# Performance work log

Measured on AMD Instinct MI355X. Metric: run time of the kernel, lower is better.

## Reference

```python
import jax, jax.numpy as jnp
import numpy as np

VOCAB, BLOCK, C, H, L = 65, 60, 384, 6, 6
HS = C // H  # 64
EPS = 1e-5


def _ln(x, g, b):
    mu = jnp.mean(x, axis=-1, keepdims=True)
    var = jnp.mean(jnp.square(x - mu), axis=-1, keepdims=True)
    return (x - mu) * jax.lax.rsqrt(var + EPS) * g + b


def setup_inputs() -> dict:
    key = jax.random.key(0)
    ks = jax.random.split(key, 16)
    std = 0.02
    B, T = 2048, 60
    inp = {
        'context': jax.random.randint(ks[0], (B, T), 0, VOCAB),
        'tok_emb': std * jax.random.normal(ks[1], (VOCAB, C), jnp.float32),
        'pos_emb': std * jax.random.normal(ks[2], (BLOCK, C), jnp.float32),
        # per-head projections stacked: [L, H, C, HS]
        'wq': std * jax.random.normal(ks[3], (L, H, C, HS), jnp.float32),
        'wk': std * jax.random.normal(ks[4], (L, H, C, HS), jnp.float32),
        'wv': std * jax.random.normal(ks[5], (L, H, C, HS), jnp.float32),
        'wo': std * jax.random.normal(ks[6], (L, C, C), jnp.float32),
        'bo': jnp.zeros((L, C), jnp.float32),
        'ln1_g': jnp.ones((L, C), jnp.float32),
        'ln1_b': jnp.zeros((L, C), jnp.float32),
        'ln2_g': jnp.ones((L, C), jnp.float32),
        'ln2_b': jnp.zeros((L, C), jnp.float32),
        'w1': std * jax.random.normal(ks[7], (L, C, 4 * C), jnp.float32),
        'b1': jnp.zeros((L, 4 * C), jnp.float32),
        'w2': std * jax.random.normal(ks[8], (L, 4 * C, C), jnp.float32),
        'b2': jnp.zeros((L, C), jnp.float32),
        'lnf_g': jnp.ones((C,), jnp.float32),
        'lnf_b': jnp.zeros((C,), jnp.float32),
        'lm_w': std * jax.random.normal(ks[9], (C, VOCAB), jnp.float32),
        'lm_b': jnp.zeros((VOCAB,), jnp.float32),
    }
    return inp


def _forward(context, tok_emb, pos_emb, wq, wk, wv, wo, bo,
             ln1_g, ln1_b, ln2_g, ln2_b, w1, b1, w2, b2,
             lnf_g, lnf_b, lm_w, lm_b):
    B, T = context.shape
    x = tok_emb[context] + pos_emb[:T]  # [B,T,C]
    causal = jnp.tril(jnp.ones((T, T), bool))
    neg_inf = jnp.finfo(x.dtype).min

    def block(x, p):
        (wq_l, wk_l, wv_l, wo_l, bo_l, g1, b1n, g2, b2n, w1_l, bb1, w2_l, bb2) = p
        h = _ln(x, g1, b1n)
        q = jnp.einsum('btc,hcd->bhtd', h, wq_l)
        k = jnp.einsum('btc,hcd->bhtd', h, wk_l)
        v = jnp.einsum('btc,hcd->bhtd', h, wv_l)
        scores = jnp.einsum('bhtd,bhsd->bhts', q, k) * (HS ** -0.5)
        scores = jnp.where(causal, scores, neg_inf)
        probs = jax.nn.softmax(scores, axis=-1)
        o = jnp.einsum('bhts,bhsd->bhtd', probs, v)
        o = o.transpose(0, 2, 1, 3).reshape(B, T, C)  # concat heads
        x = x + o @ wo_l + bo_l
        h = _ln(x, g2, b2n)
        x = x + jax.nn.relu(h @ w1_l + bb1) @ w2_l + bb2
        return x, None

    params = (wq, wk, wv, wo, bo, ln1_g, ln1_b, ln2_g, ln2_b, w1, b1, w2, b2)
    x, _ = jax.lax.scan(block, x, params)
    x = _ln(x, lnf_g, lnf_b)
    return x @ lm_w + lm_b  # [B,T,VOCAB]


def reference(context, tok_emb, pos_emb, wq, wk, wv, wo, bo,
              ln1_g, ln1_b, ln2_g, ln2_b, w1, b1, w2, b2,
              lnf_g, lnf_b, lm_w, lm_b):
    return _forward(context, tok_emb, pos_emb, wq, wk, wv, wo, bo,
                    ln1_g, ln1_b, ln2_g, ln2_b, w1, b1, w2, b2,
                    lnf_g, lnf_b, lm_w, lm_b)
```

## Files before the change

kernel.cpp:

```cpp
#include <hip/hip_runtime.h>


#define B_  2048
#define T_  60
#define C_  384
#define H_  6
#define HS_ 64
#define L_  6
#define FF_ 1536
#define V_  65

typedef unsigned int  u32;
typedef unsigned short u16;
typedef short bf16x8 __attribute__((ext_vector_type(8)));
typedef float f32x4  __attribute__((ext_vector_type(4)));

__device__ __forceinline__ float bf2f(u32 u) {
  return __uint_as_float(u << 16);
}
__device__ __forceinline__ u16 f2bf(float f) {
  u32 u = __float_as_uint(f);
  u = u + 0x7FFFu + ((u >> 16) & 1u);
  return (u16)(u >> 16);
}

typedef const __attribute__((address_space(1))) unsigned int gas_u32;
typedef __attribute__((address_space(3))) unsigned int las_u32;
__device__ __forceinline__ void gload16(const u16* g, u16* l) {
  __builtin_amdgcn_global_load_lds((gas_u32*)g, (las_u32*)l, 16, 0, 0);
}

__global__ void tconv_k(const float* __restrict__ src, u16* __restrict__ dst,
                        int K, int N, long srcStride, int nH, long sL, long sH)
{
  __shared__ float t[32][33];
  int z = blockIdx.z;
  int l = z / nH, hh = z % nH;
  const float* s = src + (long)z * srcStride;
  u16* d = dst + l * sL + hh * sH;
  int n0 = blockIdx.x * 32, k0 = blockIdx.y * 32;
  for (int yy = threadIdx.y; yy < 32; yy += 8) {
    int k = k0 + yy, n = n0 + threadIdx.x;
    t[yy][threadIdx.x] = (k < K && n < N) ? s[(long)k * N + n] : 0.f;
  }
  __syncthreads();
  for (int yy = threadIdx.y; yy < 32; yy += 8) {
    int n = n0 + yy, k = k0 + threadIdx.x;
    if (n < N && k < K) d[(long)n * K + k] = f2bf(t[threadIdx.x][yy]);
  }
}

__global__ __launch_bounds__(256) void embed_k(const int* __restrict__ ctx,
    const float* __restrict__ tok, const float* __restrict__ pos,
    float* __restrict__ x)
{
  int idx = blockIdx.x * 256 + threadIdx.x;
  int row = idx / (C_ / 4);
  int c   = (idx % (C_ / 4)) * 4;
  int t   = row % T_;
  int tk  = ctx[row];
  float4 a = *(const float4*)(tok + (long)tk * C_ + c);
  float4 p = *(const float4*)(pos + (long)t  * C_ + c);
  float4 o = make_float4(a.x + p.x, a.y + p.y, a.z + p.z, a.w + p.w);
  *(float4*)(x + (long)idx * 4) = o;
}

__global__ __launch_bounds__(256) void ln_k(const float* __restrict__ x,
    const float* __restrict__ g, const float* __restrict__ b,
    u16* __restrict__ h)
{
  int lane = threadIdx.x & 63;
  int wv   = threadIdx.x >> 6;
  long row = (long)blockIdx.x * 4 + wv;
  const float* xr = x + row * C_;
  int c0 = lane * 6;
  float v0[6];
  #pragma unroll
  for (int i = 0; i < 6; i++) v0[i] = xr[c0 + i];
  float s = 0.f, sq = 0.f;
  #pragma unroll
  for (int i = 0; i < 6; i++) { s += v0[i]; sq += v0[i] * v0[i]; }
  #pragma unroll
  for (int off = 32; off > 0; off >>= 1) {
    s  += __shfl_xor(s,  off, 64);
    sq += __shfl_xor(sq, off, 64);
  }
  float mu  = s * (1.f / C_);
  float var = sq * (1.f / C_) - mu * mu;
  float rs  = rsqrtf(var + 1e-5f);
  u16* hr = h + row * C_;
  #pragma unroll
  for (int i = 0; i < 6; i++) {
    float hv = (v0[i] - mu) * rs * g[c0 + i] + b[c0 + i];
    hr[c0 + i] = f2bf(hv);
  }
}

template<int RELU, int RES, int OBF>
__global__ __launch_bounds__(512) void gemm128g(const u16* __restrict__ A,
    const u16* __restrict__ Wt, const float* __restrict__ bias,
    const float* __restrict__ resid, void* __restrict__ outp,
    int N, int K, int mT, int nT)
{
  __shared__ __align__(16) u16 As[2][128][4][8];
  __shared__ __align__(16) u16 Bs[2][128][4][8];
  int tid = threadIdx.x;
  int bid = blockIdx.x;
  int mtile, ntile;
  if ((mT & 7) == 0) {
    int xcd = bid & 7, loc = bid >> 3;
    int q = loc / nT;
    mtile = xcd * (mT >> 3) + q;
    ntile = loc - q * nT;
  } else {
    int q = bid / nT;
    mtile = q;
    ntile = bid - q * nT;
  }
  long mBase = (long)mtile * 128;
  int  nBase = ntile * 128;
  int lane = tid & 63, wv = tid >> 6;
  int l15 = lane & 15, l4 = lane >> 4;
  int wr = wv >> 1, wc = wv & 1;
  int srow = tid >> 2;
  int seg  = (tid & 3) ^ ((tid >> 4) & 3);
  const u16* aL = A  + (mBase + srow) * (long)K + seg * 8;
  const u16* bL = Wt + ((long)nBase + srow) * K + seg * 8;
  u16* aD0 = &As[0][wv << 4][0][0];
  u16* bD0 = &Bs[0][wv << 4][0][0];
  u16* aD1 = &As[1][wv << 4][0][0];
  u16* bD1 = &Bs[1][wv << 4][0][0];
  int swR = l4 ^ (l15 >> 2);

  f32x4 acc[2][4];
  #pragma unroll
  for (int i = 0; i < 2; i++)
    #pragma unroll
    for (int j = 0; j < 4; j++)
      acc[i][j] = (f32x4){0.f, 0.f, 0.f, 0.f};

  gload16(aL, aD0);
  gload16(bL, bD0);
  __syncthreads();

  int cur = 0;
  for (int k0 = 0; k0 < K; k0 += 32) {
    if (k0 + 32 < K) {
      gload16(aL + k0 + 32, cur ? aD0 : aD1);
      gload16(bL + k0 + 32, cur ? bD0 : bD1);
    }
    bf16x8 af[2], bfr[4];
    #pragma unroll
    for (int i = 0; i < 2; i++)
      af[i] = *(const bf16x8*)&As[cur][wr * 32 + i * 16 + l15][swR][0];
    #pragma unroll
    for (int j = 0; j < 4; j++)
      bfr[j] = *(const bf16x8*)&Bs[cur][wc * 64 + j * 16 + l15][swR][0];
    #pragma unroll
    for (int i = 0; i < 2; i++)
      #pragma unroll
      for (int j = 0; j < 4; j++)
        acc[i][j] = __builtin_amdgcn_mfma_f32_16x16x32_bf16(
            af[i], bfr[j], acc[i][j], 0, 0, 0);
    __syncthreads();
    cur ^= 1;
  }

  #pragma unroll
  for (int i = 0; i < 2; i++) {
    #pragma unroll
    for (int j = 0; j < 4; j++) {
      int n = nBase + wc * 64 + j * 16 + l15;
      float bv = bias ? bias[n] : 0.f;
      #pragma unroll
      for (int r = 0; r < 4; r++) {
        long row = mBase + wr * 32 + i * 16 + l4 * 4 + r;
        float vv = acc[i][j][r] + bv;
        if (RELU) vv = fmaxf(vv, 0.f);
        if (RES)  vv += resid[row * N + n];
        if (OBF) ((u16*)outp)[row * N + n] = f2bf(vv);
        else     ((float*)outp)[row * N + n] = vv;
      }
    }
  }
}

template<int OBF>
__global__ __launch_bounds__(256) void gemm_head(const u16* __restrict__ A,
    const u16* __restrict__ Wt, const float* __restrict__ bias,
    void* __restrict__ outp, int N, int K)
{
  __shared__ __align__(16) u16 As[128][4][8];
  __shared__ __align__(16) u16 Bs[64][4][8];
  int tid  = threadIdx.x;
  int nt   = blockIdx.x;
  int nBase = nt * 64;
  long mBase = (long)blockIdx.y * 128;
  int lane = tid & 63, wv = tid >> 6;
  int l15 = lane & 15, l4 = lane >> 4;
  int sseg = tid & 3;
  int srow = tid >> 2;
  int swW = sseg ^ ((srow >> 2) & 3);
  int swR = l4 ^ (l15 >> 2);
  const u16* a0p = A + (mBase + srow) * K + sseg * 8;
  const u16* a1p = a0p + (long)64 * K;
  bool colOK = (nBase + srow) < N;
  const u16* bp  = Wt + (long)(nBase + srow) * K + sseg * 8;

  f32x4 acc[2][4];
  #pragma unroll
  for (int i = 0; i < 2; i++)
    #pragma unroll
    for (int j = 0; j < 4; j++)
      acc[i][j] = (f32x4){0.f, 0.f, 0.f, 0.f};

  for (int k0 = 0; k0 < K; k0 += 32) {
    uint4 av0 = *(const uint4*)(a0p + k0);
    uint4 av1 = *(const uint4*)(a1p + k0);
    uint4 bv  = colOK ? *(const uint4*)(bp + k0) : make_uint4(0, 0, 0, 0);
    *(uint4*)&As[srow][swW][0]      = av0;
    *(uint4*)&As[srow + 64][swW][0] = av1;
    *(uint4*)&Bs[srow][swW][0]      = bv;
    __syncthreads();
    bf16x8 af[2], bfr[4];
    af[0] = *(const bf16x8*)&As[wv * 32 + l15][swR][0];
    af[1] = *(const bf16x8*)&As[wv * 32 + 16 + l15][swR][0];
    #pragma unroll
    for (int j = 0; j < 4; j++)
      bfr[j] = *(const bf16x8*)&Bs[j * 16 + l15][swR][0];
    #pragma unroll
    for (int i = 0; i < 2; i++)
      #pragma unroll
      for (int j = 0; j < 4; j++)
        acc[i][j] = __builtin_amdgcn_mfma_f32_16x16x32_bf16(
            af[i], bfr[j], acc[i][j], 0, 0, 0);
    __syncthreads();
  }

  #pragma unroll
  for (int i = 0; i < 2; i++) {
    #pragma unroll
    for (int j = 0; j < 4; j++) {
      int n = nBase + j * 16 + l15;
      if (n < N) {
        #pragma unroll
        for (int r = 0; r < 4; r++) {
          long row = mBase + wv * 32 + i * 16 + l4 * 4 + r;
          float vv = acc[i][j][r];
          if (bias) vv += bias[n];
          if (OBF) ((u16*)outp)[row * N + n] = f2bf(vv);
          else     ((float*)outp)[row * N + n] = vv;
        }
      }
    }
  }
}

__global__ __launch_bounds__(256) void attn_k(const u16* __restrict__ qkv,
    u16* __restrict__ ao)
{
  __shared__ __align__(16) u16 qs[64][72];
  __shared__ __align__(16) u16 ks[64][72];
  __shared__ __align__(16) u16 vT[64][72];
  __shared__ __align__(16) u16 ps[64][72];
  int tid = threadIdx.x;
  int bb = blockIdx.x / H_;
  int hh = blockIdx.x % H_;
  const u16* base = qkv + ((long)bb * T_) * 1152 + hh * HS_;

  for (int i = tid; i < 576; i += 256)
    ((uint4*)vT)[i] = make_uint4(0, 0, 0, 0);
  __syncthreads();

  for (int i = tid; i < 480; i += 256) {
    int t = i >> 3, d0 = (i & 7) << 3;
    const u16* rp = base + (long)t * 1152;
    *(uint4*)&qs[t][d0] = *(const uint4*)(rp + d0);
    *(uint4*)&ks[t][d0] = *(const uint4*)(rp + 384 + d0);
    uint4 rv = *(const uint4*)(rp + 768 + d0);
    u16 vv[8] = {(u16)(rv.x & 0xffffu), (u16)(rv.x >> 16),
                 (u16)(rv.y & 0xffffu), (u16)(rv.y >> 16),
                 (u16)(rv.z & 0xffffu), (u16)(rv.z >> 16),
                 (u16)(rv.w & 0xffffu), (u16)(rv.w >> 16)};
    #pragma unroll
    for (int m = 0; m < 8; m++) vT[d0 + m][t] = vv[m];
  }
  __syncthreads();

  int lane = tid & 63, wv = tid >> 6;
  int l15 = lane & 15, quad = lane >> 4;

  bf16x8 aq0 = *(const bf16x8*)&qs[wv * 16 + l15][quad * 8];
  bf16x8 aq1 = *(const bf16x8*)&qs[wv * 16 + l15][32 + quad * 8];
  f32x4 s[4];
  #pragma unroll
  for (int jt = 0; jt < 4; jt++) {
    bf16x8 b0 = *(const bf16x8*)&ks[jt * 16 + l15][quad * 8];
    bf16x8 b1 = *(const bf16x8*)&ks[jt * 16 + l15][32 + quad * 8];
    f32x4 a2 = (f32x4){0.f, 0.f, 0.f, 0.f};
    a2 = __builtin_amdgcn_mfma_f32_16x16x32_bf16(aq0, b0, a2, 0, 0, 0);
    a2 = __builtin_amdgcn_mfma_f32_16x16x32_bf16(aq1, b1, a2, 0, 0, 0);
    s[jt] = a2;
  }

  int rbase = wv * 16 + quad * 4;
  #pragma unroll
  for (int r = 0; r < 4; r++) {
    int row = rbase + r;
    float v0[4];
    #pragma unroll
    for (int jt = 0; jt < 4; jt++) {
      int col = jt * 16 + l15;
      float sv = s[jt][r] * 0.125f;
      v0[jt] = (col <= row) ? sv : -1e30f;
    }
    float m = fmaxf(fmaxf(v0[0], v0[1]), fmaxf(v0[2], v0[3]));
    #pragma unroll
    for (int off = 1; off < 16; off <<= 1) m = fmaxf(m, __shfl_xor(m, off, 64));
    float sum = 0.f;
    #pragma unroll
    for (int jt = 0; jt < 4; jt++) { v0[jt] = __expf(v0[jt] - m); sum += v0[jt]; }
    #pragma unroll
    for (int off = 1; off < 16; off <<= 1) sum += __shfl_xor(sum, off, 64);
    float inv = 1.f / sum;
    #pragma unroll
    for (int jt = 0; jt < 4; jt++)
      ps[row][jt * 16 + l15] = f2bf(v0[jt] * inv);
  }
  __syncthreads();

  bf16x8 ap0 = *(const bf16x8*)&ps[wv * 16 + l15][quad * 8];
  bf16x8 ap1 = *(const bf16x8*)&ps[wv * 16 + l15][32 + quad * 8];
  long obase = ((long)bb * T_) * C_ + hh * HS_;
  #pragma unroll
  for (int dt = 0; dt < 4; dt++) {
    bf16x8 b0 = *(const bf16x8*)&vT[dt * 16 + l15][quad * 8];
    bf16x8 b1 = *(const bf16x8*)&vT[dt * 16 + l15][32 + quad * 8];
    f32x4 a2 = (f32x4){0.f, 0.f, 0.f, 0.f};
    a2 = __builtin_amdgcn_mfma_f32_16x16x32_bf16(ap0, b0, a2, 0, 0, 0);
    a2 = __builtin_amdgcn_mfma_f32_16x16x32_bf16(ap1, b1, a2, 0, 0, 0);
    #pragma unroll
    for (int r = 0; r < 4; r++) {
      int row = rbase + r;
      if (row < T_)
        ao[obase + (long)row * C_ + dt * 16 + l15] = f2bf(a2[r]);
    }
  }
}

extern "C" void kernel_launch(void* const* d_in, const int* in_sizes, int n_in,
                              void* d_out, int out_size, void* d_ws, size_t ws_size,
                              hipStream_t stream)
{
  const int*   ctx  = (const int*)  d_in[0];
  const float* tok  = (const float*)d_in[1];
  const float* pos  = (const float*)d_in[2];
  const float* wq   = (const float*)d_in[3];
  const float* wk   = (const float*)d_in[4];
  const float* wv   = (const float*)d_in[5];
  const float* wo   = (const float*)d_in[6];
  const float* bo   = (const float*)d_in[7];
  const float* ln1g = (const float*)d_in[8];
  const float* ln1b = (const float*)d_in[9];
  const float* ln2g = (const float*)d_in[10];
  const float* ln2b = (const float*)d_in[11];
  const float* w1   = (const float*)d_in[12];
  const float* b1   = (const float*)d_in[13];
  const float* w2   = (const float*)d_in[14];
  const float* b2   = (const float*)d_in[15];
  const float* lnfg = (const float*)d_in[16];
  const float* lnfb = (const float*)d_in[17];
  const float* lmw  = (const float*)d_in[18];
  const float* lmb  = (const float*)d_in[19];
  float* out = (float*)d_out;

  const long nQKV = (long)L_ * H_ * C_ * HS_;
  const long nWO  = (long)L_ * C_ * C_;
  const long nW1  = (long)L_ * C_ * FF_;
  const long nLM  = (long)C_ * V_;
  u16* wqkvT = (u16*)d_ws;
  u16* woT = wqkvT + 3 * nQKV;
  u16* w1T = woT + nWO;
  u16* w2T = w1T + nW1;
  u16* lmT = w2T + nW1;
  const size_t wbytes = (size_t)(nQKV * 3 + nWO + nW1 * 2 + nLM) * 2;

  int chunkB = 32;
  {
    const int cand[] = {2048, 1024, 512, 256, 128, 64, 32};
    for (int i = 0; i < 7; i++) {
      size_t U = (size_t)cand[i] * T_ * C_ * 2;
      if (wbytes + 7 * U <= ws_size) { chunkB = cand[i]; break; }
    }
  }
  const long BTc = (long)chunkB * T_;
  char* wsb = (char*)d_ws + wbytes;
  const size_t U = (size_t)BTc * C_ * 2;
  float* x    = (float*)wsb;
  u16*   h    = (u16*)(wsb + 2 * U);
  char*  reg  = wsb + 3 * U;
  u16* qkvb = (u16*)reg;
  u16* ab   = (u16*)(reg + 3 * U);
  u16* fb   = (u16*)reg;

  {
    dim3 tb(32, 8);
    const long sL = 1152L * 384, sH = 64L * 384, sec = 384L * 384;
    tconv_k<<<dim3(2, 12, L_ * H_), tb, 0, stream>>>(wq, wqkvT,
        C_, HS_, (long)C_ * HS_, H_, sL, sH);
    tconv_k<<<dim3(2, 12, L_ * H_), tb, 0, stream>>>(wk, wqkvT + sec,
        C_, HS_, (long)C_ * HS_, H_, sL, sH);
    tconv_k<<<dim3(2, 12, L_ * H_), tb, 0, stream>>>(wv, wqkvT + 2 * sec,
        C_, HS_, (long)C_ * HS_, H_, sL, sH);
    tconv_k<<<dim3(12, 12, L_), tb, 0, stream>>>(wo, woT,
        C_, C_, (long)C_ * C_, 1, (long)C_ * C_, 0);
    tconv_k<<<dim3(48, 12, L_), tb, 0, stream>>>(w1, w1T,
        C_, FF_, (long)C_ * FF_, 1, (long)C_ * FF_, 0);
    tconv_k<<<dim3(12, 48, L_), tb, 0, stream>>>(w2, w2T,
        FF_, C_, (long)FF_ * C_, 1, (long)FF_ * C_, 0);
    tconv_k<<<dim3(3, 12, 1), tb, 0, stream>>>(lmw, lmT,
        C_, V_, (long)C_ * V_, 1, 0, 0);
  }

  const long qkvL = 1152L * 384;
  const long woL  = (long)C_ * C_;
  const long w1L  = (long)C_ * FF_;
  dim3 blk(256);
  dim3 blk5(512);
  dim3 gEmb((u32)(BTc * C_ / 4 / 256));
  dim3 gLN((u32)(BTc / 4));
  int mT = (int)(BTc / 128);
  dim3 gHd(2, (u32)(BTc / 128));
  dim3 gAt((u32)(chunkB * H_));

  for (int c0 = 0; c0 < B_; c0 += chunkB) {
    const long tok0 = (long)c0 * T_;
    const int* ctxc = ctx + tok0;
    float* outc = out + tok0 * V_;

    embed_k<<<gEmb, blk, 0, stream>>>(ctxc, tok, pos, x);

    for (int l = 0; l < L_; l++) {
      ln_k<<<gLN, blk, 0, stream>>>(x, ln1g + l * C_, ln1b + l * C_, h);
      gemm128g<0,0,1><<<dim3(mT * 9), blk5, 0, stream>>>(h, wqkvT + l * qkvL,
          nullptr, nullptr, qkvb, 1152, C_, mT, 9);
      attn_k<<<gAt, blk, 0, stream>>>(qkvb, ab);
      gemm128g<0,1,0><<<dim3(mT * 3), blk5, 0, stream>>>(ab, woT + l * woL,
          bo + l * C_, x, x, C_, C_, mT, 3);
      ln_k<<<gLN, blk, 0, stream>>>(x, ln2g + l * C_, ln2b + l * C_, h);
      gemm128g<1,0,1><<<dim3(mT * 12), blk5, 0, stream>>>(h, w1T + l * w1L,
          b1 + l * FF_, nullptr, fb, FF_, C_, mT, 12);
      gemm128g<0,1,0><<<dim3(mT * 3), blk5, 0, stream>>>(fb, w2T + l * w1L,
          b2 + l * C_, x, x, C_, FF_, mT, 3);
    }

    ln_k<<<gLN, blk, 0, stream>>>(x, lnfg, lnfb, h);
    gemm_head<0><<<gHd, blk, 0, stream>>>(h, lmT, lmb, outc, V_, C_);
  }
}
```

Baseline: 5.584 ms.

## Triple-buffer GEMM LDS tiles with one barrier per K-step

```diff
diff --git a/kernel.cpp b/kernel.cpp
--- a/kernel.cpp
+++ b/kernel.cpp
@@ -97,13 +97,13 @@
 }
 
 template<int RELU, int RES, int OBF>
-__global__ __launch_bounds__(512) void gemm128g(const u16* __restrict__ A,
+__global__ __launch_bounds__(512) void gemm128p(const u16* __restrict__ A,
     const u16* __restrict__ Wt, const float* __restrict__ bias,
     const float* __restrict__ resid, void* __restrict__ outp,
     int N, int K, int mT, int nT)
 {
-  __shared__ __align__(16) u16 As[2][128][4][8];
-  __shared__ __align__(16) u16 Bs[2][128][4][8];
+  __shared__ __align__(16) u16 As[3][128][4][8];
+  __shared__ __align__(16) u16 Bs[3][128][4][8];
   int tid = threadIdx.x;
   int bid = blockIdx.x;
   int mtile, ntile;
@@ -126,11 +126,16 @@
   int seg  = (tid & 3) ^ ((tid >> 4) & 3);
   const u16* aL = A  + (mBase + srow) * (long)K + seg * 8;
   const u16* bL = Wt + ((long)nBase + srow) * K + seg * 8;
-  u16* aD0 = &As[0][wv << 4][0][0];
-  u16* bD0 = &Bs[0][wv << 4][0][0];
-  u16* aD1 = &As[1][wv << 4][0][0];
-  u16* bD1 = &Bs[1][wv << 4][0][0];
-  int swR = l4 ^ (l15 >> 2);
+  int wvOff = wv << 9;
+  u16* a0 = &As[0][0][0][0];
+  u16* a1 = &As[1][0][0][0];
+  u16* a2 = &As[2][0][0][0];
+  u16* b0 = &Bs[0][0][0][0];
+  u16* b1 = &Bs[1][0][0][0];
+  u16* b2 = &Bs[2][0][0][0];
+  int swR  = l4 ^ (l15 >> 2);
+  int aOff = ((wr * 32 + l15) * 4 + swR) * 8;
+  int bOff = ((wc * 64 + l15) * 4 + swR) * 8;
 
   f32x4 acc[2][4];
   #pragma unroll
@@ -139,31 +144,36 @@
     for (int j = 0; j < 4; j++)
       acc[i][j] = (f32x4){0.f, 0.f, 0.f, 0.f};
 
-  gload16(aL, aD0);
-  gload16(bL, bD0);
-  __syncthreads();
-
-  int cur = 0;
-  for (int k0 = 0; k0 < K; k0 += 32) {
-    if (k0 + 32 < K) {
-      gload16(aL + k0 + 32, cur ? aD0 : aD1);
-      gload16(bL + k0 + 32, cur ? bD0 : bD1);
+  const int NT = K >> 5;
+  gload16(aL,      a0 + wvOff);
+  gload16(bL,      b0 + wvOff);
+  gload16(aL + 32, a1 + wvOff);
+  gload16(bL + 32, b1 + wvOff);
+
+  for (int t = 0; t < NT; ++t) {
+    if (t + 1 < NT)
+      asm volatile("s_waitcnt vmcnt(2) lgkmcnt(0)\n\ts_barrier" ::: "memory");
+    else
+      asm volatile("s_waitcnt vmcnt(0) lgkmcnt(0)\n\ts_barrier" ::: "memory");
+    int k2 = (t + 2) << 5;
+    if (k2 < K) {
+      gload16(aL + k2, a2 + wvOff);
+      gload16(bL + k2, b2 + wvOff);
     }
     bf16x8 af[2], bfr[4];
-    #pragma unroll
-    for (int i = 0; i < 2; i++)
-      af[i] = *(const bf16x8*)&As[cur][wr * 32 + i * 16 + l15][swR][0];
+    af[0] = *(const bf16x8*)(a0 + aOff);
+    af[1] = *(const bf16x8*)(a0 + aOff + 512);
     #pragma unroll
     for (int j = 0; j < 4; j++)
-      bfr[j] = *(const bf16x8*)&Bs[cur][wc * 64 + j * 16 + l15][swR][0];
+      bfr[j] = *(const bf16x8*)(b0 + bOff + j * 512);
     #pragma unroll
     for (int i = 0; i < 2; i++)
       #pragma unroll
       for (int j = 0; j < 4; j++)
         acc[i][j] = __builtin_amdgcn_mfma_f32_16x16x32_bf16(
             af[i], bfr[j], acc[i][j], 0, 0, 0);
-    __syncthreads();
-    cur ^= 1;
+    u16* tA = a0; a0 = a1; a1 = a2; a2 = tA;
+    u16* tB = b0; b0 = b1; b1 = b2; b2 = tB;
   }
 
   #pragma unroll
@@ -442,15 +452,15 @@
 
     for (int l = 0; l < L_; l++) {
       ln_k<<<gLN, blk, 0, stream>>>(x, ln1g + l * C_, ln1b + l * C_, h);
-      gemm128g<0,0,1><<<dim3(mT * 9), blk5, 0, stream>>>(h, wqkvT + l * qkvL,
+      gemm128p<0,0,1><<<dim3(mT * 9), blk5, 0, stream>>>(h, wqkvT + l * qkvL,
           nullptr, nullptr, qkvb, 1152, C_, mT, 9);
       attn_k<<<gAt, blk, 0, stream>>>(qkvb, ab);
-      gemm128g<0,1,0><<<dim3(mT * 3), blk5, 0, stream>>>(ab, woT + l * woL,
+      gemm128p<0,1,0><<<dim3(mT * 3), blk5, 0, stream>>>(ab, woT + l * woL,
           bo + l * C_, x, x, C_, C_, mT, 3);
       ln_k<<<gLN, blk, 0, stream>>>(x, ln2g + l * C_, ln2b + l * C_, h);
-      gemm128g<1,0,1><<<dim3(mT * 12), blk5, 0, stream>>>(h, w1T + l * w1L,
+      gemm128p<1,0,1><<<dim3(mT * 12), blk5, 0, stream>>>(h, w1T + l * w1L,
           b1 + l * FF_, nullptr, fb, FF_, C_, mT, 12);
-      gemm128g<0,1,0><<<dim3(mT * 3), blk5, 0, stream>>>(fb, w2T + l * w1L,
+      gemm128p<0,1,0><<<dim3(mT * 3), blk5, 0, stream>>>(fb, w2T + l * w1L,
           b2 + l * C_, x, x, C_, FF_, mT, 3);
     }
 
```

Result: no change. 5.669 ms (+1.5%).

## Fuse residual-add GEMMs with following LayerNorm into a full-row GEMM kernel

Applied to the files above, without the earlier changes.

```diff
diff --git a/kernel.cpp b/kernel.cpp
--- a/kernel.cpp
+++ b/kernel.cpp
@@ -29,6 +29,7 @@
 __device__ __forceinline__ void gload16(const u16* g, u16* l) {
   __builtin_amdgcn_global_load_lds((gas_u32*)g, (las_u32*)l, 16, 0, 0);
 }
+#define MFMA16(a, b, c) __builtin_amdgcn_mfma_f32_16x16x32_bf16((a), (b), (c), 0, 0, 0)
 
 __global__ void tconv_k(const float* __restrict__ src, u16* __restrict__ dst,
                         int K, int N, long srcStride, int nH, long sL, long sH)
@@ -183,6 +184,124 @@
       }
     }
   }
+}
+
+__global__ __launch_bounds__(512) void gemm_ln(const u16* __restrict__ A,
+    const u16* __restrict__ Wt, const float* __restrict__ bias,
+    const float* __restrict__ g, const float* __restrict__ b,
+    float* __restrict__ x, u16* __restrict__ hout, int K, int mT)
+{
+  __shared__ __align__(16) u16 aBuf[2][2048];
+  __shared__ __align__(16) u16 bBuf[2][12288];
+  __shared__ float psum[64][4][2];
+  int tid = threadIdx.x;
+  int bid = blockIdx.x;
+  int mtile;
+  if ((mT & 7) == 0) { int xcd = bid & 7; mtile = xcd * (mT >> 3) + (bid >> 3); }
+  else mtile = bid;
+  long mBase = (long)mtile * 64;
+  int lane = tid & 63, w = tid >> 6;
+  int l15 = lane & 15, l4 = lane >> 4;
+  int wr = w >> 2, wc = w & 3;
+  int srow = tid >> 2;
+  int seg  = (tid & 3) ^ ((tid >> 4) & 3);
+  const u16* aL = A  + (mBase + (srow & 63)) * (long)K + seg * 8;
+  const u16* bL = Wt + (long)srow * K + seg * 8;
+  int swR = l4 ^ (l15 >> 2);
+  int aOff = (wr * 32 + l15) * 32 + swR * 8;
+  int bOff = (wc * 96 + l15) * 32 + swR * 8;
+
+  f32x4 acc[2][6];
+  #pragma unroll
+  for (int i = 0; i < 2; i++)
+    #pragma unroll
+    for (int j = 0; j < 6; j++)
+      acc[i][j] = (f32x4){0.f, 0.f, 0.f, 0.f};
+
+  if (w < 4) gload16(aL, &aBuf[0][w << 9]);
+  #pragma unroll
+  for (int j = 0; j < 3; j++)
+    gload16(bL + (long)j * 128 * K, &bBuf[0][j * 4096 + (w << 9)]);
+  __syncthreads();
+
+  int cur = 0;
+  for (int k0 = 0; k0 < K; k0 += 32) {
+    if (k0 + 32 < K) {
+      if (w < 4) gload16(aL + k0 + 32, &aBuf[cur ^ 1][w << 9]);
+      #pragma unroll
+      for (int j = 0; j < 3; j++)
+        gload16(bL + (long)j * 128 * K + k0 + 32,
+                &bBuf[cur ^ 1][j * 4096 + (w << 9)]);
+    }
+    bf16x8 af[2], bf[6];
+    #pragma unroll
+    for (int i = 0; i < 2; i++)
+      af[i] = *(const bf16x8*)&aBuf[cur][aOff + i * 512];
+    #pragma unroll
+    for (int j = 0; j < 6; j++)
+      bf[j] = *(const bf16x8*)&bBuf[cur][bOff + j * 512];
+    #pragma unroll
+    for (int i = 0; i < 2; i++)
+      #pragma unroll
+      for (int j = 0; j < 6; j++)
+        acc[i][j] = MFMA16(af[i], bf[j], acc[i][j]);
+    __syncthreads();
+    cur ^= 1;
+  }
+
+  #pragma unroll
+  for (int j = 0; j < 6; j++) {
+    int n = wc * 96 + j * 16 + l15;
+    float bv = bias[n];
+    #pragma unroll
+    for (int i = 0; i < 2; i++)
+      #pragma unroll
+      for (int r = 0; r < 4; r++) {
+        long rowg = mBase + wr * 32 + i * 16 + l4 * 4 + r;
+        acc[i][j][r] += bv + x[rowg * 384 + n];
+      }
+  }
+  #pragma unroll
+  for (int i = 0; i < 2; i++)
+    #pragma unroll
+    for (int r = 0; r < 4; r++) {
+      float s = 0.f, sq = 0.f;
+      #pragma unroll
+      for (int j = 0; j < 6; j++) {
+        float vv = acc[i][j][r];
+        s += vv; sq += vv * vv;
+      }
+      #pragma unroll
+      for (int off = 1; off < 16; off <<= 1) {
+        s  += __shfl_xor(s,  off, 64);
+        sq += __shfl_xor(sq, off, 64);
+      }
+      if (l15 == 0) {
+        int row = wr * 32 + i * 16 + l4 * 4 + r;
+        psum[row][wc][0] = s;
+        psum[row][wc][1] = sq;
+      }
+    }
+  __syncthreads();
+  #pragma unroll
+  for (int i = 0; i < 2; i++)
+    #pragma unroll
+    for (int r = 0; r < 4; r++) {
+      int row = wr * 32 + i * 16 + l4 * 4 + r;
+      float s  = psum[row][0][0] + psum[row][1][0] + psum[row][2][0] + psum[row][3][0];
+      float sq = psum[row][0][1] + psum[row][1][1] + psum[row][2][1] + psum[row][3][1];
+      float mu  = s * (1.f / 384.f);
+      float var = sq * (1.f / 384.f) - mu * mu;
+      float rs  = rsqrtf(var + 1e-5f);
+      long rowg = mBase + row;
+      #pragma unroll
+      for (int j = 0; j < 6; j++) {
+        int n = wc * 96 + j * 16 + l15;
+        float vv = acc[i][j][r];
+        x[rowg * 384 + n] = vv;
+        hout[rowg * 384 + n] = f2bf((vv - mu) * rs * g[n] + b[n]);
+      }
+    }
 }
 
 template<int OBF>
@@ -397,10 +516,9 @@
   char* wsb = (char*)d_ws + wbytes;
   const size_t U = (size_t)BTc * C_ * 2;
   float* x    = (float*)wsb;
-  u16*   h    = (u16*)(wsb + 2 * U);
+  u16*   hab  = (u16*)(wsb + 2 * U);
   char*  reg  = wsb + 3 * U;
   u16* qkvb = (u16*)reg;
-  u16* ab   = (u16*)(reg + 3 * U);
   u16* fb   = (u16*)reg;
 
   {
@@ -429,7 +547,8 @@
   dim3 blk5(512);
   dim3 gEmb((u32)(BTc * C_ / 4 / 256));
   dim3 gLN((u32)(BTc / 4));
-  int mT = (int)(BTc / 128);
+  int mT   = (int)(BTc / 128);
+  int mT64 = (int)(BTc / 64);
   dim3 gHd(2, (u32)(BTc / 128));
   dim3 gAt((u32)(chunkB * H_));
 
@@ -439,22 +558,22 @@
     float* outc = out + tok0 * V_;
 
     embed_k<<<gEmb, blk, 0, stream>>>(ctxc, tok, pos, x);
+    ln_k<<<gLN, blk, 0, stream>>>(x, ln1g, ln1b, hab);
 
     for (int l = 0; l < L_; l++) {
-      ln_k<<<gLN, blk, 0, stream>>>(x, ln1g + l * C_, ln1b + l * C_, h);
-      gemm128g<0,0,1><<<dim3(mT * 9), blk5, 0, stream>>>(h, wqkvT + l * qkvL,
+      gemm128g<0,0,1><<<dim3(mT * 9), blk5, 0, stream>>>(hab, wqkvT + l * qkvL,
           nullptr, nullptr, qkvb, 1152, C_, mT, 9);
-      attn_k<<<gAt, blk, 0, stream>>>(qkvb, ab);
-      gemm128g<0,1,0><<<dim3(mT * 3), blk5, 0, stream>>>(ab, woT + l * woL,
-          bo + l * C_, x, x, C_, C_, mT, 3);
-      ln_k<<<gLN, blk, 0, stream>>>(x, ln2g + l * C_, ln2b + l * C_, h);
-      gemm128g<1,0,1><<<dim3(mT * 12), blk5, 0, stream>>>(h, w1T + l * w1L,
+      attn_k<<<gAt, blk, 0, stream>>>(qkvb, hab);
+      gemm_ln<<<dim3(mT64), blk5, 0, stream>>>(hab, woT + l * woL,
+          bo + l * C_, ln2g + l * C_, ln2b + l * C_, x, hab, C_, mT64);
+      gemm128g<1,0,1><<<dim3(mT * 12), blk5, 0, stream>>>(hab, w1T + l * w1L,
           b1 + l * FF_, nullptr, fb, FF_, C_, mT, 12);
-      gemm128g<0,1,0><<<dim3(mT * 3), blk5, 0, stream>>>(fb, w2T + l * w1L,
-          b2 + l * C_, x, x, C_, FF_, mT, 3);
-    }
-
-    ln_k<<<gLN, blk, 0, stream>>>(x, lnfg, lnfb, h);
-    gemm_head<0><<<gHd, blk, 0, stream>>>(h, lmT, lmb, outc, V_, C_);
-  }
-}
+      const float* gg = (l < L_ - 1) ? (ln1g + (l + 1) * C_) : lnfg;
+      const float* bb = (l < L_ - 1) ? (ln1b + (l + 1) * C_) : lnfb;
+      gemm_ln<<<dim3(mT64), blk5, 0, stream>>>(fb, w2T + l * w1L,
+          b2 + l * C_, gg, bb, x, hab, FF_, mT64);
+    }
+
+    gemm_head<0><<<gHd, blk, 0, stream>>>(hab, lmT, lmb, outc, V_, C_);
+  }
+}
```

Result: no change. 5.482 ms (-1.8%).
